# Kernel tuning notes

Hardware: AMD Instinct MI355X
Metric: run time of the kernel (lower is better)

The kernel has to match this reference:

```python
import jax, jax.numpy as jnp
import numpy as np
import math

B, L, D = 2, 2048, 1024
H, T, F = 16, 4, 4096
DK = D // H
EPS = 1e-5


def setup_inputs() -> dict:
    key = jax.random.key(0)
    ks = jax.random.split(key, 20)
    s = 0.02
    inp = {
        "x": jax.random.normal(ks[0], (B, L, D), jnp.float32),
        "token_types": jax.random.randint(ks[1], (B, L), 0, 4, jnp.int32),
        "seq_lens": jax.random.randint(ks[2], (B,), L // 2, L + 1, jnp.int32),
        "Wq": jax.random.normal(ks[3], (D, D), jnp.float32) * s,
        "Wk": jax.random.normal(ks[4], (D, D), jnp.float32) * s,
        "Wv": jax.random.normal(ks[5], (D, D), jnp.float32) * s,
        "Wu": jax.random.normal(ks[6], (D, D), jnp.float32) * s,
        "Wo": jax.random.normal(ks[7], (D, D), jnp.float32) * s,
        "ln1_g": jnp.ones((T, D), jnp.float32),
        "ln1_b": jnp.zeros((T, D), jnp.float32),
        "W1": jax.random.normal(ks[8], (T, D, F), jnp.float32) * s,
        "b1": jnp.zeros((T, F), jnp.float32),
        "W2": jax.random.normal(ks[9], (T, F, D), jnp.float32) * s,
        "b2": jnp.zeros((T, D), jnp.float32),
        "ln2_g": jnp.ones((T, D), jnp.float32),
        "ln2_b": jnp.zeros((T, D), jnp.float32),
    }
    return inp


def _token_ln(x, g, b, token_types):
    # normalization is identical across types; only gamma/beta differ per type
    mu = jnp.mean(x, axis=-1, keepdims=True)
    var = jnp.mean(jnp.square(x - mu), axis=-1, keepdims=True)
    xn = (x - mu) / jnp.sqrt(var + EPS)
    return xn * g[token_types] + b[token_types]


def _hstu_attn(x, token_types, seq_lens, Wq, Wk, Wv, Wu, Wo):
    neg = jnp.finfo(x.dtype).min
    Q = (x @ Wq).reshape(B, L, H, DK)
    K = (x @ Wk).reshape(B, L, H, DK)
    V = (x @ Wv).reshape(B, L, H, DK)
    U = (x @ Wu).reshape(B, L, H, DK)
    scores = jnp.einsum('blhd,bmhd->bhlm', Q, K) / math.sqrt(DK)  # [B,H,L,L]
    # hybrid mask: allow j<=i (causal) OR key j is a prompt token (type<3)
    is_prompt_j = (token_types < 3)[:, None, :]                    # [B,1,L]
    causal_ok = jnp.tril(jnp.ones((L, L), bool))[None]             # [1,L,L]
    allow = causal_ok | is_prompt_j                                 # [B,L,L]
    scores = scores + jnp.where(allow, 0.0, neg)[:, None]
    # padding mask on keys
    pad = jnp.arange(L)[None, :] >= seq_lens[:, None]               # [B,L]
    scores = jnp.where(pad[:, None, None, :], neg, scores)
    attn = jax.nn.softmax(scores, axis=-1)
    out = jnp.einsum('bhlm,bmhd->blhd', attn, V) * U                # U-gating
    return out.reshape(B, L, D) @ Wo


def _token_ffn(x, token_types, W1, b1, W2, b2):
    out = jnp.zeros_like(x)
    for t in range(T):  # fixed small number of token types
        h = jax.nn.gelu(x @ W1[t] + b1[t], approximate=False) @ W2[t] + b2[t]
        out = out + jnp.where((token_types == t)[..., None], h, 0.0)
    return out


def reference(x, token_types, seq_lens, Wq, Wk, Wv, Wu, Wo,
              ln1_g, ln1_b, W1, b1, W2, b2, ln2_g, ln2_b):
    h = _hstu_attn(x, token_types, seq_lens, Wq, Wk, Wv, Wu, Wo)
    x = _token_ln(x + h, ln1_g, ln1_b, token_types)
    h = _token_ffn(x, token_types, W1, b1, W2, b2)
    x = _token_ln(x + h, ln2_g, ln2_b, token_types)
    return x
```

## Files before the change

### kernel.cpp

```cpp
#include <hip/hip_runtime.h>
#include <hip/hip_bf16.h>
#include <math.h>

#define B_   2
#define L_   2048
#define D_   1024
#define H_   16
#define DK_  64
#define T_   4
#define F_   4096
#define NTOK (B_ * L_)

typedef __bf16 bf16_t;
typedef bf16_t bf16x8 __attribute__((ext_vector_type(8)));
typedef float  f32x4  __attribute__((ext_vector_type(4)));
typedef unsigned short u16;
typedef u16 u16x8 __attribute__((ext_vector_type(8)));
typedef unsigned long long ull;

static __device__ __forceinline__ u16 f2b(float f) {
    __hip_bfloat16 h = __float2bfloat16(f);
    return *reinterpret_cast<u16*>(&h);
}
static __device__ __forceinline__ float b2f(u16 u) {
    __hip_bfloat16 h;
    *reinterpret_cast<u16*>(&h) = u;
    return __bfloat162float(h);
}

static __device__ __forceinline__ void gld16(void* lds, const void* g) {
    __builtin_amdgcn_global_load_lds(
        (const __attribute__((address_space(1))) unsigned int*)g,
        (__attribute__((address_space(3))) unsigned int*)lds,
        16, 0, 0);
}

#define VMW(N) do { asm volatile("s_waitcnt vmcnt(" #N ")" ::: "memory"); \
                    __builtin_amdgcn_sched_barrier(0); } while (0)
#define BARR() do { __builtin_amdgcn_sched_barrier(0); \
                    __builtin_amdgcn_s_barrier();      \
                    __builtin_amdgcn_sched_barrier(0); } while (0)

__global__ void k_cast_bf16(const float* __restrict__ in, u16* __restrict__ out, int n4) {
    int i = blockIdx.x * 256 + threadIdx.x;
    if (i >= n4) return;
    float4 v = reinterpret_cast<const float4*>(in)[i];
    ushort4 o;
    o.x = f2b(v.x); o.y = f2b(v.y); o.z = f2b(v.z); o.w = f2b(v.w);
    reinterpret_cast<ushort4*>(out)[i] = o;
}

__global__ void k_tcast(const float* __restrict__ W, u16* __restrict__ Wt,
                        int K, int N, long sW, long sWt) {
    __shared__ float tile[32][33];
    int z = blockIdx.z;
    W  += (long)z * sW;
    Wt += (long)z * sWt;
    int n0 = blockIdx.x * 32, k0 = blockIdx.y * 32;
    int tx = threadIdx.x, ty = threadIdx.y;
#pragma unroll
    for (int i = 0; i < 4; i++)
        tile[ty + 8 * i][tx] = W[(long)(k0 + ty + 8 * i) * N + n0 + tx];
    __syncthreads();
#pragma unroll
    for (int i = 0; i < 4; i++)
        Wt[(long)(n0 + ty + 8 * i) * K + k0 + tx] = f2b(tile[tx][ty + 8 * i]);
}

enum { EP_BF16 = 0, EP_F32 = 1, EP_GELU_BF16 = 2, EP_BIAS_F32 = 3 };

#define RRG 8192

#define CLUSTER(BB, KK)  do {                                                   \
    bf16x8 bv[4], av[4];                                                        \
    _Pragma("unroll")                                                           \
    for (int n = 0; n < 4; n++)                                                 \
        bv[n] = *reinterpret_cast<const bf16x8*>((BB) + regB + offB[n][KK]);    \
    _Pragma("unroll")                                                           \
    for (int m = 0; m < 4; m++)                                                 \
        av[m] = *reinterpret_cast<const bf16x8*>((BB) + offA[m][KK]);           \
    __builtin_amdgcn_s_setprio(1);                                              \
    _Pragma("unroll")                                                           \
    for (int m = 0; m < 4; m++)                                                 \
        _Pragma("unroll")                                                       \
        for (int n = 0; n < 4; n++)                                             \
            acc[0][m][n] = __builtin_amdgcn_mfma_f32_16x16x32_bf16(             \
                av[m], bv[n], acc[0][m][n], 0, 0, 0);                           \
    __builtin_amdgcn_s_setprio(0);                                              \
    _Pragma("unroll")                                                           \
    for (int m = 0; m < 4; m++)                                                 \
        av[m] = *reinterpret_cast<const bf16x8*>((BB) + RRG + offA[m][KK]);     \
    __builtin_amdgcn_s_setprio(1);                                              \
    _Pragma("unroll")                                                           \
    for (int m = 0; m < 4; m++)                                                 \
        _Pragma("unroll")                                                       \
        for (int n = 0; n < 4; n++)                                             \
            acc[1][m][n] = __builtin_amdgcn_mfma_f32_16x16x32_bf16(             \
                av[m], bv[n], acc[1][m][n], 0, 0, 0);                           \
    __builtin_amdgcn_s_setprio(0);                                              \
} while (0)

template <int MODE, bool AIDX, bool CIDX, bool GROUPED, int KS, bool VTOUT>
__global__ __launch_bounds__(512, 1)
void k_g2(const u16* __restrict__ A, const u16* __restrict__ Bt,
          void* __restrict__ Cv, float* __restrict__ Cpart, long partStride,
          u16* __restrict__ VTbuf,
          const float* __restrict__ bias,
          const int* __restrict__ idxb, const int* __restrict__ boff,
          const int* __restrict__ bcnt,
          int M, int K, int lda, int ldb, int ldc,
          long strideB, int biasStride)
{
    const int ks = (KS > 1) ? (int)blockIdx.z : 0;
    int kBeg = 0, kEnd = K;
    if (KS > 1) {
        int Kc = ((K / KS) + 63) & ~63;
        kBeg = ks * Kc;
        kEnd = min(K, kBeg + Kc);
    }
    const int gx = gridDim.x;
    const int nwg = gx * gridDim.y;
    const int id = blockIdx.y * gx + blockIdx.x;
    const int q8 = nwg >> 3, r8 = nwg & 7, xcd = id & 7, sub = id >> 3;
    const int id2 = (xcd < r8 ? xcd * (q8 + 1) : r8 * (q8 + 1) + (xcd - r8) * q8) + sub;
    const int tm = id2 % gx, tn = id2 / gx;
    const int bm = tm * 256, bn = tn * 256;

    int pend = M;
    if (GROUPED) {
        bool dead = true;
        int g = 0;
#pragma unroll
        for (int t = 0; t < T_; t++) {
            int o = boff[t], c = bcnt[t];
            int pe = o + (((c + 255) >> 8) << 8);
            if (bm >= o && bm < pe) { g = t; pend = o + c; dead = false; }
        }
        if (dead) return;
        Bt += (long)g * strideB;
        bias += (long)g * biasStride;
    }

    const int tid = threadIdx.x;
    const int wid = tid >> 6, lane = tid & 63;
    const int lg = lane >> 4, lr = lane & 15;
    const int wr = wid >> 2, wc = wid & 3;

    __shared__ u16 lds[8 * RRG];

    const int srow = tid >> 3;
    const int soff = ((tid & 7) ^ (srow & 7)) * 8;
    const u16* pAr[4];
    const u16* pBr[4];
#pragma unroll
    for (int j = 0; j < 4; j++) {
        int pa = bm + srow + j * 64;
        if (GROUPED) pa = min(pa, pend - 1);
        long ra = AIDX ? (long)idxb[pa] : (long)pa;
        pAr[j] = A + ra * lda + kBeg + soff;
        pBr[j] = Bt + (long)(bn + srow + j * 64) * ldb + kBeg + soff;
    }
    auto STAGE1 = [&](u16* dn, long ko) {
        gld16(dn + 0 * RRG + tid * 8,        pAr[0] + ko);
        gld16(dn + 0 * RRG + (512 + tid) * 8, pAr[1] + ko);
        gld16(dn + 2 * RRG + tid * 8,        pBr[0] + ko);
        gld16(dn + 2 * RRG + (512 + tid) * 8, pBr[1] + ko);
    };
    auto STAGE2 = [&](u16* dn, long ko) {
        gld16(dn + 1 * RRG + tid * 8,        pAr[2] + ko);
        gld16(dn + 1 * RRG + (512 + tid) * 8, pAr[3] + ko);
        gld16(dn + 3 * RRG + tid * 8,        pBr[2] + ko);
        gld16(dn + 3 * RRG + (512 + tid) * 8, pBr[3] + ko);
    };

    int offA[4][2], offB[4][2];
    const int regB = (2 + (wc >> 1)) * RRG;
#pragma unroll
    for (int i = 0; i < 4; i++) {
        int raf = wr * 64 + i * 16 + lr;
        int rbf = (wc & 1) * 64 + i * 16 + lr;
#pragma unroll
        for (int k = 0; k < 2; k++) {
            offA[i][k] = raf * 64 + (((lg + 4 * k) ^ (raf & 7)) * 8);
            offB[i][k] = rbf * 64 + (((lg + 4 * k) ^ (rbf & 7)) * 8);
        }
    }

    const f32x4 zero = {0.f, 0.f, 0.f, 0.f};
    f32x4 acc[2][4][4];
#pragma unroll
    for (int qa = 0; qa < 2; qa++)
#pragma unroll
        for (int m = 0; m < 4; m++)
#pragma unroll
            for (int n = 0; n < 4; n++) acc[qa][m][n] = zero;

    const int NT = (kEnd - kBeg) >> 6;

    STAGE1(lds, 0);
    STAGE2(lds, 0);

    for (int t = 0; t < NT; t++) {
        u16* bb_ = lds + (t & 1) * 4 * RRG;
        u16* dn  = lds + ((t & 1) ^ 1) * 4 * RRG;
        const long ko = (long)(t + 1) * 64;
        if (t + 1 < NT) {
            STAGE1(dn, ko);
            VMW(4);
        } else {
            VMW(0);
        }
        BARR();
        CLUSTER(bb_, 0);
        if (t + 1 < NT) STAGE2(dn, ko);
        CLUSTER(bb_, 1);
        BARR();
    }

    if (VTOUT && bn >= 2048 && bn < 3072) {
#pragma unroll
        for (int qa = 0; qa < 2; qa++) {
#pragma unroll
            for (int m = 0; m < 4; m++) {
                int tok0 = bm + qa * 128 + wr * 64 + m * 16 + lg * 4;
                int bb2 = tok0 >> 11, tin = tok0 & 2047;
#pragma unroll
                for (int n = 0; n < 4; n++) {
                    int gn = bn + wc * 64 + n * 16 + lr;
                    int d = gn - 2048, hh = d >> 6, dk = d & 63;
                    ushort4 o4;
                    o4.x = f2b(acc[qa][m][n][0]); o4.y = f2b(acc[qa][m][n][1]);
                    o4.z = f2b(acc[qa][m][n][2]); o4.w = f2b(acc[qa][m][n][3]);
                    long vi = ((long)(bb2 * 16 + hh) * 64 + dk) * 2048 + tin;
                    *reinterpret_cast<ushort4*>(VTbuf + vi) = o4;
                }
            }
        }
        return;
    }
#pragma unroll
    for (int qa = 0; qa < 2; qa++) {
#pragma unroll
        for (int m = 0; m < 4; m++) {
#pragma unroll
            for (int r = 0; r < 4; r++) {
                int prow = bm + qa * 128 + wr * 64 + m * 16 + lg * 4 + r;
                if (GROUPED && prow >= pend) continue;
                long crow = CIDX ? (long)idxb[prow] : (long)prow;
#pragma unroll
                for (int n = 0; n < 4; n++) {
                    int gn = bn + wc * 64 + n * 16 + lr;
                    float v = acc[qa][m][n][r];
                    long off = crow * (long)ldc + gn;
                    if (KS > 1 && ks > 0) {
                        Cpart[(long)(ks - 1) * partStride + off] = v;
                    } else {
                        if (MODE == EP_GELU_BF16) {
                            v += bias[gn];
                            v = 0.5f * v * (1.0f + erff(v * 0.70710678118654752f));
                        }
                        if (MODE == EP_BIAS_F32) v += bias[gn];
                        if (MODE == EP_BF16 || MODE == EP_GELU_BF16)
                            ((u16*)Cv)[off] = f2b(v);
                        else
                            ((float*)Cv)[off] = v;
                    }
                }
            }
        }
    }
}

#define KVB 128
__global__ __launch_bounds__(256)
void k_attn(const u16* __restrict__ cat, const u16* __restrict__ VT,
            const int* __restrict__ types, const int* __restrict__ seql,
            u16* __restrict__ AG)
{
    const int qt = blockIdx.x, h = blockIdx.y, b = blockIdx.z;
    const int tid = threadIdx.x, w = tid >> 6, lane = tid & 63;
    const int lg = lane >> 4, lr = lane & 15;
    const int qbase = qt * 64;

    __shared__ u16 sK[KVB * 64];
    __shared__ u16 sV[64 * KVB];
    __shared__ u16 sP[4 * 16 * KVB];
    __shared__ ull smask[4];

    const int seqlen = seql[b];
    const float QSC = 0.125f * 1.44269504f;
    const u16* vtb = VT + (long)(b * 16 + h) * 64 * 2048;

    const long qrow = (long)(b * L_ + qbase + w * 16 + lr);
    const u16* qp = cat + qrow * 4096 + h * 64;
    bf16x8 qf0, qf1;
    {
        u16x8 a0 = *reinterpret_cast<const u16x8*>(qp + lg * 8);
        u16x8 a1 = *reinterpret_cast<const u16x8*>(qp + 32 + lg * 8);
#pragma unroll
        for (int e = 0; e < 8; e++) {
            qf0[e] = (bf16_t)(b2f(a0[e]) * QSC);
            qf1[e] = (bf16_t)(b2f(a1[e]) * QSC);
        }
    }

    const f32x4 zero = {0.f, 0.f, 0.f, 0.f};
    f32x4 o[4] = {zero, zero, zero, zero};
    float mrow[4] = {-1e30f, -1e30f, -1e30f, -1e30f};
    float lsum[4] = {0.f, 0.f, 0.f, 0.f};

    for (int kb = 0; kb < L_; kb += KVB) {
        if (kb >= seqlen) break;
#pragma unroll
        for (int i = 0; i < 4; i++) {
            int c = tid + 256 * i;
            int row = c >> 3, sl = (c & 7) ^ (row & 7);
            gld16(sK + c * 8, cat + (long)(b * L_ + kb + row) * 4096 + 1024 + h * 64 + sl * 8);
        }
#pragma unroll
        for (int i = 0; i < 4; i++) {
            int c = tid + 256 * i;
            int row = c >> 4, ch = c & 15;
            int sl = ch ^ (row & 15);
            gld16(sV + c * 8, vtb + (long)row * 2048 + kb + sl * 8);
        }
        if (w < 2) {
            int j = kb + w * 64 + lane;
            ull pm = __ballot(j >= seqlen);
            ull rm = __ballot(types[b * L_ + j] < 3);
            if (lane == 0) { smask[w * 2] = pm; smask[w * 2 + 1] = rm; }
        }
        __syncthreads();
        const ull pad0 = smask[0], pr0 = smask[1], pad1 = smask[2], pr1 = smask[3];

        f32x4 s[8];
#pragma unroll
        for (int n = 0; n < 8; n++) {
            int row = n * 16 + lr, r7 = row & 7;
            bf16x8 bk0 = *reinterpret_cast<const bf16x8*>(sK + row * 64 + ((lg ^ r7)) * 8);
            bf16x8 bk1 = *reinterpret_cast<const bf16x8*>(sK + row * 64 + (((lg ^ 4)) ^ r7) * 8);
            f32x4 t4 = zero;
            t4 = __builtin_amdgcn_mfma_f32_16x16x32_bf16(qf0, bk0, t4, 0, 0, 0);
            t4 = __builtin_amdgcn_mfma_f32_16x16x32_bf16(qf1, bk1, t4, 0, 0, 0);
            s[n] = t4;
        }

        float tmax[4] = {-1e30f, -1e30f, -1e30f, -1e30f};
        const bool interior = (kb + KVB <= qbase) && (kb + KVB <= seqlen);
        const bool future   = (kb > qbase + 63);
        if (interior) {
#pragma unroll
            for (int n = 0; n < 8; n++)
#pragma unroll
                for (int r = 0; r < 4; r++) tmax[r] = fmaxf(tmax[r], s[n][r]);
        } else if (future) {
            const ull d0 = pad0 | ~pr0, d1 = pad1 | ~pr1;
#pragma unroll
            for (int n = 0; n < 8; n++) {
                bool dead = (((n < 4) ? d0 : d1) >> (((n & 3) * 16 + lr))) & 1ull;
#pragma unroll
                for (int r = 0; r < 4; r++) {
                    float sv = dead ? -1e30f : s[n][r];
                    s[n][r] = sv;
                    tmax[r] = fmaxf(tmax[r], sv);
                }
            }
        } else {
            ull dm0[4], dm1[4];
#pragma unroll
            for (int r = 0; r < 4; r++) {
                int d = qbase + w * 16 + 4 * lg + r - kb;
                ull h0 = (d < 0) ? ~0ull : ((d >= 63) ? 0ull : (~0ull << (d + 1)));
                ull h1 = (d < 64) ? ~0ull : ((d >= 127) ? 0ull : (~0ull << (d - 63)));
                dm0[r] = pad0 | (~pr0 & h0);
                dm1[r] = pad1 | (~pr1 & h1);
            }
#pragma unroll
            for (int n = 0; n < 8; n++) {
                int bp = (n & 3) * 16 + lr;
#pragma unroll
                for (int r = 0; r < 4; r++) {
                    bool dead = (((n < 4) ? dm0[r] : dm1[r]) >> bp) & 1ull;
                    float sv = dead ? -1e30f : s[n][r];
                    s[n][r] = sv;
                    tmax[r] = fmaxf(tmax[r], sv);
                }
            }
        }
#pragma unroll
        for (int r = 0; r < 4; r++) {
#pragma unroll
            for (int d = 1; d < 16; d <<= 1)
                tmax[r] = fmaxf(tmax[r], __shfl_xor(tmax[r], d, 64));
        }
        bool grew = (tmax[0] > mrow[0]) || (tmax[1] > mrow[1]) ||
                    (tmax[2] > mrow[2]) || (tmax[3] > mrow[3]);
        if (__any(grew)) {
            float corr[4];
#pragma unroll
            for (int r = 0; r < 4; r++) {
                float mnew = fmaxf(mrow[r], tmax[r]);
                corr[r] = __builtin_amdgcn_exp2f(mrow[r] - mnew);
                mrow[r] = mnew;
                lsum[r] *= corr[r];
            }
#pragma unroll
            for (int n2 = 0; n2 < 4; n2++) {
                f32x4 t4 = o[n2];
#pragma unroll
                for (int r = 0; r < 4; r++) t4[r] *= corr[r];
                o[n2] = t4;
            }
        }
        float rsum[4] = {0.f, 0.f, 0.f, 0.f};
#pragma unroll
        for (int n = 0; n < 8; n++)
#pragma unroll
            for (int r = 0; r < 4; r++) {
                float p = __builtin_amdgcn_exp2f(s[n][r] - mrow[r]);
                s[n][r] = p;
                rsum[r] += p;
            }
#pragma unroll
        for (int r = 0; r < 4; r++) {
#pragma unroll
            for (int d = 1; d < 16; d <<= 1) rsum[r] += __shfl_xor(rsum[r], d, 64);
            lsum[r] += rsum[r];
        }
        u16* Pw = sP + w * (16 * KVB);
#pragma unroll
        for (int n = 0; n < 8; n++) {
            int pc = n * 2 + (lr >> 3), p7 = lr & 7;
#pragma unroll
            for (int r = 0; r < 4; r++) {
                int q = 4 * lg + r;
                Pw[q * KVB + (pc ^ q) * 8 + p7] = f2b(s[n][r]);
            }
        }
        bf16x8 pa[4];
#pragma unroll
        for (int st = 0; st < 4; st++)
            pa[st] = *reinterpret_cast<const bf16x8*>(Pw + lr * KVB + ((st * 4 + lg) ^ lr) * 8);
#pragma unroll
        for (int n2 = 0; n2 < 4; n2++) {
            int row = n2 * 16 + lr, r15 = row & 15;
            f32x4 t4 = o[n2];
#pragma unroll
            for (int st = 0; st < 4; st++) {
                bf16x8 vb = *reinterpret_cast<const bf16x8*>(sV + row * KVB + ((st * 4 + lg) ^ r15) * 8);
                t4 = __builtin_amdgcn_mfma_f32_16x16x32_bf16(pa[st], vb, t4, 0, 0, 0);
            }
            o[n2] = t4;
        }
        __syncthreads();
    }
#pragma unroll
    for (int n2 = 0; n2 < 4; n2++) {
#pragma unroll
        for (int r = 0; r < 4; r++) {
            int ig = qbase + w * 16 + 4 * lg + r;
            long orow = (long)(b * L_ + ig);
            int j = n2 * 16 + lr;
            float u = b2f(cat[orow * 4096 + 3072 + h * 64 + j]);
            float val = o[n2][r] / lsum[r] * u;
            AG[orow * 1024 + h * 64 + j] = f2b(val);
        }
    }
}

template <bool WB, int NP>
__global__ __launch_bounds__(256)
void k_ln(const float* __restrict__ xa, const float* __restrict__ ha,
          const float* __restrict__ p1, const float* __restrict__ p2,
          const float* __restrict__ p3,
          const float* __restrict__ g, const float* __restrict__ bb,
          const int* __restrict__ types,
          float* __restrict__ of, u16* __restrict__ ob)
{
    const int tok = blockIdx.x, tid = threadIdx.x;
    const long base = (long)tok * D_;
    float4 va = reinterpret_cast<const float4*>(xa + base)[tid];
    float4 vh = reinterpret_cast<const float4*>(ha + base)[tid];
    if (NP >= 2) {
        float4 a = reinterpret_cast<const float4*>(p1 + base)[tid];
        float4 c = reinterpret_cast<const float4*>(p2 + base)[tid];
        vh.x += a.x + c.x; vh.y += a.y + c.y; vh.z += a.z + c.z; vh.w += a.w + c.w;
    }
    if (NP >= 3) {
        float4 a = reinterpret_cast<const float4*>(p3 + base)[tid];
        vh.x += a.x; vh.y += a.y; vh.z += a.z; vh.w += a.w;
    }
    float v0 = va.x + vh.x, v1 = va.y + vh.y, v2 = va.z + vh.z, v3 = va.w + vh.w;
    float s = v0 + v1 + v2 + v3;
    float ss = v0 * v0 + v1 * v1 + v2 * v2 + v3 * v3;
#pragma unroll
    for (int d = 1; d < 64; d <<= 1) { s += __shfl_xor(s, d, 64); ss += __shfl_xor(ss, d, 64); }
    __shared__ float red[8];
    if ((tid & 63) == 0) { red[tid >> 6] = s; red[4 + (tid >> 6)] = ss; }
    __syncthreads();
    s  = red[0] + red[1] + red[2] + red[3];
    ss = red[4] + red[5] + red[6] + red[7];
    const float mu  = s * (1.f / D_);
    const float var = ss * (1.f / D_) - mu * mu;
    const float inv = rsqrtf(var + 1e-5f);
    const int t = types[tok];
    const float* gp = g + (long)t * D_ + tid * 4;
    const float* bp = bb + (long)t * D_ + tid * 4;
    float o0 = (v0 - mu) * inv * gp[0] + bp[0];
    float o1 = (v1 - mu) * inv * gp[1] + bp[1];
    float o2 = (v2 - mu) * inv * gp[2] + bp[2];
    float o3 = (v3 - mu) * inv * gp[3] + bp[3];
    reinterpret_cast<float4*>(of + base)[tid] = make_float4(o0, o1, o2, o3);
    if (WB) {
        ushort4 u4;
        u4.x = f2b(o0); u4.y = f2b(o1); u4.z = f2b(o2); u4.w = f2b(o3);
        reinterpret_cast<ushort4*>(ob + base)[tid] = u4;
    }
}

__global__ void k_count(const int* __restrict__ types, int* __restrict__ cnt) {
    int i = blockIdx.x * 256 + threadIdx.x;
    if (i < NTOK) atomicAdd(&cnt[types[i]], 1);
}
__global__ void k_scan(int* __restrict__ base) {
    if (threadIdx.x == 0) {
        int a = 0;
        for (int t = 0; t < T_; t++) {
            base[4 + t] = a;
            base[8 + t] = a;
            a += ((base[t] + 255) >> 8) << 8;
        }
    }
}
__global__ void k_fill(const int* __restrict__ types, int* __restrict__ cur, int* __restrict__ idxb) {
    int i = blockIdx.x * 256 + threadIdx.x;
    if (i < NTOK) {
        int p = atomicAdd(&cur[types[i]], 1);
        idxb[p] = i;
    }
}

extern "C" void kernel_launch(void* const* d_in, const int* in_sizes, int n_in,
                              void* d_out, int out_size, void* d_ws, size_t ws_size,
                              hipStream_t stream) {
    const float* x    = (const float*)d_in[0];
    const int* types  = (const int*)d_in[1];
    const int* seql   = (const int*)d_in[2];
    const float* Wq   = (const float*)d_in[3];
    const float* Wk   = (const float*)d_in[4];
    const float* Wv   = (const float*)d_in[5];
    const float* Wu   = (const float*)d_in[6];
    const float* Wo   = (const float*)d_in[7];
    const float* ln1g = (const float*)d_in[8];
    const float* ln1b = (const float*)d_in[9];
    const float* W1   = (const float*)d_in[10];
    const float* b1   = (const float*)d_in[11];
    const float* W2   = (const float*)d_in[12];
    const float* b2   = (const float*)d_in[13];
    const float* ln2g = (const float*)d_in[14];
    const float* ln2b = (const float*)d_in[15];

    char* ws = (char*)d_ws;
    constexpr size_t OFF_WT  = 0;
    constexpr size_t OFF_WOT = OFF_WT  + (size_t)4096 * 1024 * 2;
    constexpr size_t OFF_W1T = OFF_WOT + (size_t)1024 * 1024 * 2;
    constexpr size_t OFF_W2T = OFF_W1T + (size_t)T_ * 4096 * 1024 * 2;
    constexpr size_t OFF_XB  = OFF_W2T + (size_t)T_ * 4096 * 1024 * 2;
    constexpr size_t OFF_CAT = OFF_XB  + (size_t)NTOK * D_ * 2;
    constexpr size_t OFF_H   = OFF_CAT + (size_t)NTOK * 4096 * 2;
    constexpr size_t OFF_X1  = OFF_H   + (size_t)NTOK * D_ * 4;
    constexpr size_t OFF_X1B = OFF_X1  + (size_t)NTOK * D_ * 4;
    constexpr size_t OFF_INT = OFF_X1B + (size_t)NTOK * D_ * 2;

    u16* WT   = (u16*)(ws + OFF_WT);
    u16* WOT  = (u16*)(ws + OFF_WOT);
    u16* W1T  = (u16*)(ws + OFF_W1T);
    u16* W2T  = (u16*)(ws + OFF_W2T);
    u16* XB   = (u16*)(ws + OFF_XB);
    u16* CAT  = (u16*)(ws + OFF_CAT);
    float* Hb = (float*)(ws + OFF_H);
    u16* VT   = (u16*)(ws + OFF_H);
    float* X1 = (float*)(ws + OFF_X1);
    u16* X1B  = (u16*)(ws + OFF_X1B);
    float* PkF = (float*)(ws + OFF_W1T);
    float* PkW = (float*)(ws + OFF_CAT);
    int* ibase = (int*)(ws + OFF_INT);
    int* cnt = ibase, *off = ibase + 4, *cur = ibase + 8, *idxb = ibase + 16;

    dim3 blk(256), blk512(512), tb(32, 8);
    const long PSTR = (long)NTOK * D_;
    const int MT_PAD = 20;

    k_cast_bf16<<<NTOK * D_ / 4 / 256, blk, 0, stream>>>(x, XB, NTOK * D_ / 4);
    k_tcast<<<dim3(32, 32, 1), tb, 0, stream>>>(Wq, WT + 0 * 1048576, 1024, 1024, 0, 0);
    k_tcast<<<dim3(32, 32, 1), tb, 0, stream>>>(Wk, WT + 1 * 1048576, 1024, 1024, 0, 0);
    k_tcast<<<dim3(32, 32, 1), tb, 0, stream>>>(Wv, WT + 2 * 1048576, 1024, 1024, 0, 0);
    k_tcast<<<dim3(32, 32, 1), tb, 0, stream>>>(Wu, WT + 3 * 1048576, 1024, 1024, 0, 0);
    k_tcast<<<dim3(32, 32, 1), tb, 0, stream>>>(Wo, WOT, 1024, 1024, 0, 0);
    k_tcast<<<dim3(128, 32, T_), tb, 0, stream>>>(W1, W1T, 1024, 4096, (long)1024 * 4096, (long)4096 * 1024);
    k_tcast<<<dim3(32, 128, T_), tb, 0, stream>>>(W2, W2T, 4096, 1024, (long)4096 * 1024, (long)1024 * 4096);

    k_g2<EP_BF16, false, false, false, 1, true><<<dim3(16, 16), blk512, 0, stream>>>(
        XB, WT, CAT, nullptr, 0, VT, nullptr, nullptr, nullptr, nullptr,
        NTOK, 1024, 1024, 1024, 4096, 0, 0);

    k_attn<<<dim3(L_ / 64, H_, B_), blk, 0, stream>>>(CAT, VT, types, seql, XB);

    k_g2<EP_F32, false, false, false, 3, false><<<dim3(16, 4, 3), blk512, 0, stream>>>(
        XB, WOT, Hb, PkW, PSTR, nullptr, nullptr, nullptr, nullptr, nullptr,
        NTOK, 1024, 1024, 1024, 1024, 0, 0);

    k_ln<true, 2><<<NTOK, blk, 0, stream>>>(x, Hb, PkW, PkW + PSTR, nullptr,
                                            ln1g, ln1b, types, X1, X1B);

    hipMemsetAsync(cnt, 0, 48, stream);
    k_count<<<NTOK / 256, blk, 0, stream>>>(types, cnt);
    k_scan<<<1, 64, 0, stream>>>(ibase);
    k_fill<<<NTOK / 256, blk, 0, stream>>>(types, cur, idxb);

    k_g2<EP_GELU_BF16, true, false, true, 1, false><<<dim3(MT_PAD, 16), blk512, 0, stream>>>(
        X1B, W1T, CAT, nullptr, 0, nullptr, b1, idxb, off, cnt,
        NTOK, 1024, 1024, 1024, 4096, (long)4096 * 1024, 4096);

    k_g2<EP_BIAS_F32, false, true, true, 3, false><<<dim3(MT_PAD, 4, 3), blk512, 0, stream>>>(
        CAT, W2T, Hb, PkF, PSTR, nullptr, b2, idxb, off, cnt,
        NTOK, 4096, 4096, 4096, 1024, (long)1024 * 4096, 1024);

    k_ln<false, 2><<<NTOK, blk, 0, stream>>>(X1, Hb, PkF, PkF + PSTR, nullptr,
                                             ln2g, ln2b, types, (float*)d_out, nullptr);
}
```

Baseline: 453.7 us.

## Restructure GEMM main loop into four barrier-separated phases with staggered prefetch

Rewrites the 256x256 bf16 GEMM inner loop into four phases, each computing one quadrant of the warp's tile between barriers. Global-to-LDS loads for the next tile are spread across the phases, and B is prefetched two tiles ahead into the current buffer. The warp-to-row mapping changes so each warp owns 128 contiguous rows, and each phase reloads only half of A or B from LDS. This adds more barriers per iteration and cuts register pressure from fragments, in exchange for finer overlap of loads with MFMA work.

```diff
diff --git a/kernel.cpp b/kernel.cpp
--- a/kernel.cpp
+++ b/kernel.cpp
@@ -71,33 +71,30 @@
 
 #define RRG 8192
 
-#define CLUSTER(BB, KK)  do {                                                   \
-    bf16x8 bv[4], av[4];                                                        \
-    _Pragma("unroll")                                                           \
-    for (int n = 0; n < 4; n++)                                                 \
-        bv[n] = *reinterpret_cast<const bf16x8*>((BB) + regB + offB[n][KK]);    \
-    _Pragma("unroll")                                                           \
-    for (int m = 0; m < 4; m++)                                                 \
-        av[m] = *reinterpret_cast<const bf16x8*>((BB) + offA[m][KK]);           \
+#define LDA(MQ) do {                                                            \
+    _Pragma("unroll") for (int m = 0; m < 4; m++)                               \
+    _Pragma("unroll") for (int kk = 0; kk < 2; kk++)                            \
+        av[m][kk] = *reinterpret_cast<const bf16x8*>(                           \
+            bb_ + regA + ((MQ) * 64 + m * 16 + lr) * 64 + cko[kk]);             \
+} while (0)
+
+#define LDB(NQ, BV) do {                                                        \
+    _Pragma("unroll") for (int n = 0; n < 2; n++)                               \
+    _Pragma("unroll") for (int kk = 0; kk < 2; kk++)                            \
+        BV[n][kk] = *reinterpret_cast<const bf16x8*>(                           \
+            bb_ + regB + ((wc & 1) * 64 + (NQ) * 32 + n * 16 + lr) * 64 + cko[kk]); \
+} while (0)
+
+#define PH(MQ, NQ, BV) do {                                                     \
+    BARR();                                                                     \
     __builtin_amdgcn_s_setprio(1);                                              \
-    _Pragma("unroll")                                                           \
-    for (int m = 0; m < 4; m++)                                                 \
-        _Pragma("unroll")                                                       \
-        for (int n = 0; n < 4; n++)                                             \
-            acc[0][m][n] = __builtin_amdgcn_mfma_f32_16x16x32_bf16(             \
-                av[m], bv[n], acc[0][m][n], 0, 0, 0);                           \
+    _Pragma("unroll") for (int m = 0; m < 4; m++)                               \
+    _Pragma("unroll") for (int kk = 0; kk < 2; kk++)                            \
+    _Pragma("unroll") for (int n = 0; n < 2; n++)                               \
+        acc[MQ][NQ][m][n] = __builtin_amdgcn_mfma_f32_16x16x32_bf16(            \
+            av[m][kk], BV[n][kk], acc[MQ][NQ][m][n], 0, 0, 0);                  \
     __builtin_amdgcn_s_setprio(0);                                              \
-    _Pragma("unroll")                                                           \
-    for (int m = 0; m < 4; m++)                                                 \
-        av[m] = *reinterpret_cast<const bf16x8*>((BB) + RRG + offA[m][KK]);     \
-    __builtin_amdgcn_s_setprio(1);                                              \
-    _Pragma("unroll")                                                           \
-    for (int m = 0; m < 4; m++)                                                 \
-        _Pragma("unroll")                                                       \
-        for (int n = 0; n < 4; n++)                                             \
-            acc[1][m][n] = __builtin_amdgcn_mfma_f32_16x16x32_bf16(             \
-                av[m], bv[n], acc[1][m][n], 0, 0, 0);                           \
-    __builtin_amdgcn_s_setprio(0);                                              \
+    BARR();                                                                     \
 } while (0)
 
 template <int MODE, bool AIDX, bool CIDX, bool GROUPED, int KS, bool VTOUT>
@@ -160,110 +157,123 @@
         pAr[j] = A + ra * lda + kBeg + soff;
         pBr[j] = Bt + (long)(bn + srow + j * 64) * ldb + kBeg + soff;
     }
-    auto STAGE1 = [&](u16* dn, long ko) {
-        gld16(dn + 0 * RRG + tid * 8,        pAr[0] + ko);
-        gld16(dn + 0 * RRG + (512 + tid) * 8, pAr[1] + ko);
-        gld16(dn + 2 * RRG + tid * 8,        pBr[0] + ko);
-        gld16(dn + 2 * RRG + (512 + tid) * 8, pBr[1] + ko);
+    auto STH = [&](u16* dn, int reg, const u16* p0, const u16* p1, long ko) {
+        gld16(dn + reg * RRG + tid * 8,         p0 + ko);
+        gld16(dn + reg * RRG + (512 + tid) * 8, p1 + ko);
     };
-    auto STAGE2 = [&](u16* dn, long ko) {
-        gld16(dn + 1 * RRG + tid * 8,        pAr[2] + ko);
-        gld16(dn + 1 * RRG + (512 + tid) * 8, pAr[3] + ko);
-        gld16(dn + 3 * RRG + tid * 8,        pBr[2] + ko);
-        gld16(dn + 3 * RRG + (512 + tid) * 8, pBr[3] + ko);
-    };
-
-    int offA[4][2], offB[4][2];
+
+    const int regA = wr * RRG;
     const int regB = (2 + (wc >> 1)) * RRG;
-#pragma unroll
-    for (int i = 0; i < 4; i++) {
-        int raf = wr * 64 + i * 16 + lr;
-        int rbf = (wc & 1) * 64 + i * 16 + lr;
-#pragma unroll
-        for (int k = 0; k < 2; k++) {
-            offA[i][k] = raf * 64 + (((lg + 4 * k) ^ (raf & 7)) * 8);
-            offB[i][k] = rbf * 64 + (((lg + 4 * k) ^ (rbf & 7)) * 8);
-        }
-    }
+    int cko[2];
+#pragma unroll
+    for (int kk = 0; kk < 2; kk++) cko[kk] = ((lg + 4 * kk) ^ (lr & 7)) * 8;
 
     const f32x4 zero = {0.f, 0.f, 0.f, 0.f};
-    f32x4 acc[2][4][4];
-#pragma unroll
-    for (int qa = 0; qa < 2; qa++)
-#pragma unroll
-        for (int m = 0; m < 4; m++)
-#pragma unroll
-            for (int n = 0; n < 4; n++) acc[qa][m][n] = zero;
+    f32x4 acc[2][2][4][2];
+#pragma unroll
+    for (int mq = 0; mq < 2; mq++)
+#pragma unroll
+        for (int nq = 0; nq < 2; nq++)
+#pragma unroll
+            for (int m = 0; m < 4; m++)
+#pragma unroll
+                for (int n = 0; n < 2; n++) acc[mq][nq][m][n] = zero;
 
     const int NT = (kEnd - kBeg) >> 6;
 
-    STAGE1(lds, 0);
-    STAGE2(lds, 0);
+    STH(lds, 0, pAr[0], pAr[1], 0);
+    STH(lds, 1, pAr[2], pAr[3], 0);
+    STH(lds, 2, pBr[0], pBr[1], 0);
+    STH(lds, 3, pBr[2], pBr[3], 0);
+    if (NT > 1) {
+        u16* b1p = lds + 4 * RRG;
+        STH(b1p, 2, pBr[0], pBr[1], 64);
+        STH(b1p, 3, pBr[2], pBr[3], 64);
+        VMW(4);
+    } else {
+        VMW(0);
+    }
+    BARR();
 
     for (int t = 0; t < NT; t++) {
-        u16* bb_ = lds + (t & 1) * 4 * RRG;
-        u16* dn  = lds + ((t & 1) ^ 1) * 4 * RRG;
-        const long ko = (long)(t + 1) * 64;
-        if (t + 1 < NT) {
-            STAGE1(dn, ko);
+        const u16* bb_ = lds + (t & 1) * 4 * RRG;
+        u16* bnx = lds + ((t & 1) ^ 1) * 4 * RRG;
+        u16* bcu = lds + (t & 1) * 4 * RRG;
+        const long ko1 = (long)(t + 1) * 64, ko2 = (long)(t + 2) * 64;
+        const bool s1 = (t + 1 < NT), s2 = (t + 2 < NT);
+        bf16x8 av[4][2], bv0[2][2], bv1[2][2];
+
+        LDA(0); LDB(0, bv0);
+        if (s1) STH(bnx, 0, pAr[0], pAr[1], ko1);
+        PH(0, 0, bv0);
+        LDB(1, bv1);
+        if (s1) STH(bnx, 1, pAr[2], pAr[3], ko1);
+        PH(0, 1, bv1);
+        LDA(1);
+        if (s2) STH(bcu, 2, pBr[0], pBr[1], ko2);
+        PH(1, 1, bv1);
+        if (s2) {
+            STH(bcu, 3, pBr[2], pBr[3], ko2);
             VMW(4);
         } else {
             VMW(0);
         }
-        BARR();
-        CLUSTER(bb_, 0);
-        if (t + 1 < NT) STAGE2(dn, ko);
-        CLUSTER(bb_, 1);
-        BARR();
+        PH(1, 0, bv0);
     }
 
     if (VTOUT && bn >= 2048 && bn < 3072) {
 #pragma unroll
-        for (int qa = 0; qa < 2; qa++) {
+        for (int mq = 0; mq < 2; mq++) {
 #pragma unroll
             for (int m = 0; m < 4; m++) {
-                int tok0 = bm + qa * 128 + wr * 64 + m * 16 + lg * 4;
+                int tok0 = bm + wr * 128 + mq * 64 + m * 16 + lg * 4;
                 int bb2 = tok0 >> 11, tin = tok0 & 2047;
 #pragma unroll
-                for (int n = 0; n < 4; n++) {
-                    int gn = bn + wc * 64 + n * 16 + lr;
-                    int d = gn - 2048, hh = d >> 6, dk = d & 63;
-                    ushort4 o4;
-                    o4.x = f2b(acc[qa][m][n][0]); o4.y = f2b(acc[qa][m][n][1]);
-                    o4.z = f2b(acc[qa][m][n][2]); o4.w = f2b(acc[qa][m][n][3]);
-                    long vi = ((long)(bb2 * 16 + hh) * 64 + dk) * 2048 + tin;
-                    *reinterpret_cast<ushort4*>(VTbuf + vi) = o4;
+                for (int nq = 0; nq < 2; nq++) {
+#pragma unroll
+                    for (int n = 0; n < 2; n++) {
+                        int gn = bn + wc * 64 + nq * 32 + n * 16 + lr;
+                        int d = gn - 2048, hh = d >> 6, dk = d & 63;
+                        ushort4 o4;
+                        o4.x = f2b(acc[mq][nq][m][n][0]); o4.y = f2b(acc[mq][nq][m][n][1]);
+                        o4.z = f2b(acc[mq][nq][m][n][2]); o4.w = f2b(acc[mq][nq][m][n][3]);
+                        long vi = ((long)(bb2 * 16 + hh) * 64 + dk) * 2048 + tin;
+                        *reinterpret_cast<ushort4*>(VTbuf + vi) = o4;
+                    }
                 }
             }
         }
         return;
     }
 #pragma unroll
-    for (int qa = 0; qa < 2; qa++) {
+    for (int mq = 0; mq < 2; mq++) {
 #pragma unroll
         for (int m = 0; m < 4; m++) {
 #pragma unroll
             for (int r = 0; r < 4; r++) {
-                int prow = bm + qa * 128 + wr * 64 + m * 16 + lg * 4 + r;
+                int prow = bm + wr * 128 + mq * 64 + m * 16 + lg * 4 + r;
                 if (GROUPED && prow >= pend) continue;
                 long crow = CIDX ? (long)idxb[prow] : (long)prow;
 #pragma unroll
-                for (int n = 0; n < 4; n++) {
-                    int gn = bn + wc * 64 + n * 16 + lr;
-                    float v = acc[qa][m][n][r];
-                    long off = crow * (long)ldc + gn;
-                    if (KS > 1 && ks > 0) {
-                        Cpart[(long)(ks - 1) * partStride + off] = v;
-                    } else {
-                        if (MODE == EP_GELU_BF16) {
-                            v += bias[gn];
-                            v = 0.5f * v * (1.0f + erff(v * 0.70710678118654752f));
+                for (int nq = 0; nq < 2; nq++) {
+#pragma unroll
+                    for (int n = 0; n < 2; n++) {
+                        int gn = bn + wc * 64 + nq * 32 + n * 16 + lr;
+                        float v = acc[mq][nq][m][n][r];
+                        long off = crow * (long)ldc + gn;
+                        if (KS > 1 && ks > 0) {
+                            Cpart[(long)(ks - 1) * partStride + off] = v;
+                        } else {
+                            if (MODE == EP_GELU_BF16) {
+                                v += bias[gn];
+                                v = 0.5f * v * (1.0f + erff(v * 0.70710678118654752f));
+                            }
+                            if (MODE == EP_BIAS_F32) v += bias[gn];
+                            if (MODE == EP_BF16 || MODE == EP_GELU_BF16)
+                                ((u16*)Cv)[off] = f2b(v);
+                            else
+                                ((float*)Cv)[off] = v;
                         }
-                        if (MODE == EP_BIAS_F32) v += bias[gn];
-                        if (MODE == EP_BF16 || MODE == EP_GELU_BF16)
-                            ((u16*)Cv)[off] = f2b(v);
-                        else
-                            ((float*)Cv)[off] = v;
                     }
                 }
             }
```

New measurement: 458.2 us. No clear change (+1.0%).
